# Performance work log

Hardware: AMD Instinct MI355X
Metric: run time of the kernel (lower is better)

Reference implementation:

```python
import jax, jax.numpy as jnp
import numpy as np

H = W = 128
C = 256
NC = 15
BASE_SIZE = 8.0
SCALE = 4.0
RING = np.array([0, 1, 2, 5, 8, 7, 6, 3])  # clockwise ring of 3x3 kernel (row-major idx)
BIAS_CLS = float(-np.log((1.0 - 0.01) / 0.01))  # bias_init_with_prob(0.01)


def conv(x, w, b, pad):
    y = jax.lax.conv_general_dilated(x, w, (1, 1), [(pad, pad), (pad, pad)],
                                     dimension_numbers=('NCHW', 'OIHW', 'NCHW'))
    return y + b[None, :, None, None]


def conv_relu(x, w, b):
    return jax.nn.relu(conv(x, w, b, 1))


def gen_grid_anchors(h, w, stride):
    # AnchorGeneratorRotated: base anchor centered at 0.5*(base_size-1), shifted by stride grid
    ctr = 0.5 * (BASE_SIZE - 1.0)
    gx = jnp.arange(w, dtype=jnp.float32) * stride
    gy = jnp.arange(h, dtype=jnp.float32) * stride
    yy, xx = jnp.meshgrid(gy, gx, indexing='ij')  # row-major (y outer, x inner)
    size = BASE_SIZE * SCALE
    return jnp.stack([xx + ctr, yy + ctr,
                      jnp.full_like(xx, size), jnp.full_like(xx, size),
                      jnp.zeros_like(xx)], axis=-1).reshape(-1, 5)


def norm_angle(a):
    PI = np.pi
    return ((a + PI / 4.0) % PI) - PI / 4.0  # into [-pi/4, 3pi/4)


def rboxes_decode(anchors, deltas, wh_ratio_clip=1e-6):
    # anchors [HW,5], deltas [N,HW,5] -> [N,HW,5]
    max_ratio = float(np.abs(np.log(wh_ratio_clip)))
    dx, dy, dw, dh, dt = [deltas[..., i] for i in range(5)]
    dw = jnp.clip(dw, -max_ratio, max_ratio)
    dh = jnp.clip(dh, -max_ratio, max_ratio)
    ax, ay, aw, ah, aa = [anchors[..., i] for i in range(5)]
    cos, sin = jnp.cos(aa), jnp.sin(aa)
    gx = dx * aw * cos - dy * ah * sin + ax
    gy = dx * aw * sin + dy * ah * cos + ay
    gw = aw * jnp.exp(dw)
    gh = ah * jnp.exp(dh)
    ga = norm_angle(aa + dt)
    return jnp.stack([gx, gy, gw, gh, ga], axis=-1)


def bilinear_sample(x, ys, xs):
    # x [N,C,H,W]; ys/xs [N,H,W,K] float pixel coords -> [N,C,H,W,K], zero outside
    N, Cc, h, w = x.shape
    K = ys.shape[-1]
    x0 = jnp.floor(xs)
    y0 = jnp.floor(ys)
    wx1 = xs - x0
    wx0 = 1.0 - wx1
    wy1 = ys - y0
    wy0 = 1.0 - wy1
    xf = x.reshape(N, Cc, h * w)

    def gather(yi, wy, xi, wxx):
        valid = (yi >= 0) & (yi < h) & (xi >= 0) & (xi < w)
        yc = jnp.clip(yi, 0, h - 1).astype(jnp.int32)
        xc = jnp.clip(xi, 0, w - 1).astype(jnp.int32)
        idx = (yc * w + xc).reshape(N, -1)  # [N,H*W*K]
        v = jax.vmap(lambda xi_, ii_: jnp.take(xi_, ii_, axis=1))(xf, idx)
        v = v.reshape(N, Cc, h, w, K)
        wgt = jnp.where(valid, wy * wxx, 0.0)[:, None]  # [N,1,H,W,K]
        return v * wgt

    out = gather(y0, wy0, x0, wx0)
    out = out + gather(y0, wy0, x0 + 1.0, wx1)
    out = out + gather(y0 + 1.0, wy1, x0, wx0)
    out = out + gather(y0 + 1.0, wy1, x0 + 1.0, wx1)
    return out


def align_conv(x, refine_anchor, stride, w, b):
    # deformable 3x3 conv; sampling grid from refined rotated anchors
    N, Cc, h, ww = x.shape
    k = 3
    idx = jnp.arange(-1, 2, dtype=x.dtype)
    yy, xx = jnp.meshgrid(idx, idx, indexing='ij')
    xx = xx.reshape(-1)
    yy = yy.reshape(-1)  # [9] kernel offsets, row-major matching OIHW flatten
    axc, ayc, aw, ah, aa = [refine_anchor[..., i] for i in range(5)]
    s = jnp.asarray(stride, x.dtype)
    axc, ayc, aw, ah = axc / s, ayc / s, aw / s, ah / s
    cos, sin = jnp.cos(aa), jnp.sin(aa)
    dx = (aw / k)[..., None] * xx  # [N,h,w,9]
    dy = (ah / k)[..., None] * yy
    xs = cos[..., None] * dx - sin[..., None] * dy + axc[..., None]
    ys = sin[..., None] * dx + cos[..., None] * dy + ayc[..., None]
    sampled = bilinear_sample(x, ys, xs)  # [N,C,h,w,9]
    out = jnp.einsum('nchwk,ock->nohw', sampled, w.reshape(w.shape[0], Cc, 9))
    return jax.nn.relu(out + b[None, :, None, None])


def or_conv(x, w, b):
    # ORConv2d(256->32, arf_config=(1,8)): 8 spatially-rotated copies of each 3x3 filter
    o, ci = w.shape[0], w.shape[1]
    wf = w.reshape(o, ci, 9)
    rotated = []
    for r in range(8):
        src = np.arange(9)
        for j in range(8):
            src[RING[j]] = RING[(j - r) % 8]  # rotate ring by r*45deg, center fixed
        rotated.append(wf[..., src])
    wr = jnp.stack(rotated, axis=1).reshape(o * 8, ci, 3, 3)  # channel = o*8 + r
    br = jnp.repeat(b, 8)
    return conv(x, wr, br, 1)


def setup_inputs() -> dict:
    key = jax.random.key(0)
    ks = iter(jax.random.split(key, 32))
    d = {}
    d['feats'] = jax.random.normal(next(ks), (1, C, H, W), dtype=jnp.float32)
    def wlike(shape):
        return 0.01 * jax.random.normal(next(ks), shape, dtype=jnp.float32)
    d['fam_reg_w0'] = wlike((C, C, 3, 3)); d['fam_reg_b0'] = jnp.zeros((C,), jnp.float32)
    d['fam_reg_w1'] = wlike((C, C, 3, 3)); d['fam_reg_b1'] = jnp.zeros((C,), jnp.float32)
    d['fam_reg_hw'] = wlike((5, C, 1, 1)); d['fam_reg_hb'] = jnp.zeros((5,), jnp.float32)
    d['fam_cls_w0'] = wlike((C, C, 3, 3)); d['fam_cls_b0'] = jnp.zeros((C,), jnp.float32)
    d['fam_cls_w1'] = wlike((C, C, 3, 3)); d['fam_cls_b1'] = jnp.zeros((C,), jnp.float32)
    d['fam_cls_hw'] = wlike((NC, C, 1, 1)); d['fam_cls_hb'] = jnp.full((NC,), BIAS_CLS, jnp.float32)
    d['align_w'] = wlike((C, C, 3, 3)); d['align_b'] = jnp.zeros((C,), jnp.float32)
    d['or_w'] = wlike((C // 8, C, 3, 3)); d['or_b'] = jnp.zeros((C // 8,), jnp.float32)
    d['odm_reg_w0'] = wlike((C, C, 3, 3)); d['odm_reg_b0'] = jnp.zeros((C,), jnp.float32)
    d['odm_reg_w1'] = wlike((C, C, 3, 3)); d['odm_reg_b1'] = jnp.zeros((C,), jnp.float32)
    d['odm_reg_hw'] = wlike((5, C, 3, 3)); d['odm_reg_hb'] = jnp.zeros((5,), jnp.float32)
    d['odm_cls_w0'] = wlike((C, C // 8, 3, 3)); d['odm_cls_b0'] = jnp.zeros((C,), jnp.float32)
    d['odm_cls_w1'] = wlike((C, C, 3, 3)); d['odm_cls_b1'] = jnp.zeros((C,), jnp.float32)
    d['odm_cls_hw'] = wlike((NC, C, 3, 3)); d['odm_cls_hb'] = jnp.full((NC,), BIAS_CLS, jnp.float32)
    d['stride'] = 8
    return d


def reference(feats, fam_reg_w0, fam_reg_b0, fam_reg_w1, fam_reg_b1, fam_reg_hw, fam_reg_hb,
              fam_cls_w0, fam_cls_b0, fam_cls_w1, fam_cls_b1, fam_cls_hw, fam_cls_hb,
              align_w, align_b, or_w, or_b,
              odm_reg_w0, odm_reg_b0, odm_reg_w1, odm_reg_b1, odm_reg_hw, odm_reg_hb,
              odm_cls_w0, odm_cls_b0, odm_cls_w1, odm_cls_b1, odm_cls_hw, odm_cls_hb,
              stride):
    x = feats
    t = conv_relu(conv_relu(x, fam_reg_w0, fam_reg_b0), fam_reg_w1, fam_reg_b1)
    fam_bbox_pred = conv(t, fam_reg_hw, fam_reg_hb, 0)  # [N,5,h,w]
    t = conv_relu(conv_relu(x, fam_cls_w0, fam_cls_b0), fam_cls_w1, fam_cls_b1)
    fam_cls_pred = conv(t, fam_cls_hw, fam_cls_hb, 0)   # [N,NC,h,w]
    N, _, h, w = fam_bbox_pred.shape
    anchors = gen_grid_anchors(h, w, stride)  # [h*w,5]
    deltas = jax.lax.stop_gradient(fam_bbox_pred).transpose(0, 2, 3, 1).reshape(N, -1, 5)
    refine_anchor = rboxes_decode(anchors, deltas).reshape(N, h, w, 5)
    al = align_conv(x, refine_anchor, stride, align_w, align_b)  # [N,256,h,w]
    orf = or_conv(al, or_w, or_b)                                # [N,256,h,w]
    pooled = orf.reshape(N, -1, 8, h, w).max(axis=2)             # rotation-invariant pooling -> [N,32,h,w]
    t = conv_relu(conv_relu(pooled, odm_cls_w0, odm_cls_b0), odm_cls_w1, odm_cls_b1)
    odm_cls_pred = conv(t, odm_cls_hw, odm_cls_hb, 1)
    t = conv_relu(conv_relu(orf, odm_reg_w0, odm_reg_b0), odm_reg_w1, odm_reg_b1)
    odm_bbox_pred = conv(t, odm_reg_hw, odm_reg_hb, 1)
    return (fam_cls_pred, fam_bbox_pred, odm_cls_pred, odm_bbox_pred, anchors, refine_anchor)
```

## Files before the change

kernel.cpp:

```cpp
#include <hip/hip_runtime.h>
#include <hip/hip_bf16.h>
#include <hip/hip_fp16.h>

#define HW 128
#define NPX 16384
#define CC 256

typedef short  bf16x8  __attribute__((ext_vector_type(8)));
typedef short  short4v __attribute__((ext_vector_type(4)));
typedef float  f32x4   __attribute__((ext_vector_type(4)));
typedef unsigned int u32x4 __attribute__((ext_vector_type(4)));

static __device__ __forceinline__ short f2bs(float v) {
    union { float f; unsigned u; } x; x.f = v;
    unsigned r = x.u + 0x7FFFu + ((x.u >> 16) & 1u);
    return (short)(r >> 16);
}
static __device__ __forceinline__ float bs2f(short s) {
    union { unsigned u; float f; } x; x.u = ((unsigned)(unsigned short)s) << 16;
    return x.f;
}

struct F8 { unsigned char b; };
__device__ __forceinline__ unsigned char enc8(float v) {
// ... 63 lines not shown
    }
}

__global__ __launch_bounds__(256) void v10_prep(
    const float* __restrict__ w, const float* __restrict__ bias,
    short* __restrict__ wb, float* __restrict__ bb,
    int Cout, int Cin, int OCP, int mode)
{
    int g = blockIdx.x * 256 + threadIdx.x;
    if (g < OCP) bb[g] = (g < Cout) ? ((mode == 1) ? bias[g >> 3] : bias[g]) : 0.f;
    int tot = 9 * OCP * Cin;
    if (g >= tot) return;
    int t   = g / (OCP * Cin);
    int rem = g - t * OCP * Cin;
    int oc  = rem / Cin;
    int ci  = rem - oc * Cin;
    float v = 0.f;
    if (oc < Cout) {
        if (mode == 0)      v = w[((size_t)oc * Cin + ci) * 9 + t];
        else if (mode == 1) { int o = oc >> 3, r = oc & 7;
                              v = w[((size_t)o * Cin + ci) * 9 + c_ROT9[r][t]]; }
        else if (t == 4)    v = w[(size_t)oc * Cin + ci];
    }
    wb[g] = f2bs(v);
}

__constant__ int c_JOB[14][5] = {
    {0,       256, 256, 256, 0},
    {589824,  256, 256, 256, 0},
    {1179648, 256, 256, 256, 0},
    {1769472, 256, 256, 256, 0},
    {2359296, 256, 256, 256, 0},
    {2949120, 256, 256, 256, 1},
    {3538944, 256, 256, 256, 0},
    {4128768, 256, 256, 256, 0},
    {4718592, 256, 256, 256, 0},
    {5308416, 5,   256, 64,  2},
    {5455872, 15,  256, 64,  2},
    {5603328, 5,   256, 64,  0},
    {5750784, 15,  256, 64,  0},
    {5898240, 256, 32,  256, 0},
};

__global__ __launch_bounds__(256) void v12_prepall(
    const float* w0, const float* w1, const float* w2, const float* w3,
    const float* w4, const float* w5, const float* w6, const float* w7,
    const float* w8, const float* w9, const float* w10, const float* w11,
    const float* w12, const float* w13,
    const float* b0, const float* b1, const float* b2, const float* b3,
    const float* b4, const float* b5, const float* b6, const float* b7,
    const float* b8, const float* b9, const float* b10, const float* b11,
    const float* b12, const float* b13,
    short* __restrict__ wball, float* __restrict__ bball)
{
    const float* ws_[14] = {w0,w1,w2,w3,w4,w5,w6,w7,w8,w9,w10,w11,w12,w13};
    const float* bs_[14] = {b0,b1,b2,b3,b4,b5,b6,b7,b8,b9,b10,b11,b12,b13};
    const int j = blockIdx.y;
    const int dst  = c_JOB[j][0];
    const int Cout = c_JOB[j][1];
    const int Cin  = c_JOB[j][2];
    const int OCP  = c_JOB[j][3];
    const int mode = c_JOB[j][4];
    const float* w = ws_[j];
    const float* bias = bs_[j];
    int g = blockIdx.x * 256 + threadIdx.x;
    if (g < OCP) bball[j * 256 + g] = (g < Cout) ? ((mode == 1) ? bias[g >> 3] : bias[g]) : 0.f;
    int tot = 9 * OCP * Cin;
    if (g >= tot) return;
    int t   = g / (OCP * Cin);
    int rem = g - t * OCP * Cin;
    int oc  = rem / Cin;
    int ci  = rem - oc * Cin;
    float v = 0.f;
    if (oc < Cout) {
        if (mode == 0)      v = w[((size_t)oc * Cin + ci) * 9 + t];
        else if (mode == 1) { int o = oc >> 3, r = oc & 7;
                              v = w[((size_t)o * Cin + ci) * 9 + c_ROT9[r][t]]; }
        else if (t == 4)    v = w[(size_t)oc * Cin + ci];
    }
    wball[dst + g] = f2bs(v);
}

template <int RELU, int HEAD, int ONLY1, int CIN, int OCG>
__global__ __launch_bounds__(256) void v12_conv(
    const short* __restrict__ xin, const short* __restrict__ wb,
    const float* __restrict__ bb, void* __restrict__ outv, int CoutAct)
{
    const int OCP  = gridDim.y * 64 * OCG;
    const int y    = blockIdx.x >> 1;
    const int xh   = (blockIdx.x & 1) * 64;
    const int ocb  = blockIdx.y * 64 * OCG;
    const int tid  = threadIdx.x;
    const int wv   = tid >> 6;
    const int lane = tid & 63;
    const int quad = lane >> 4;
    const int l15  = lane & 15;
    const int ocw  = ocb + wv * 16 * OCG;

    __shared__ short S[2][3 * 66 * 40];

    int gofs[4], lofs[4];
#pragma unroll
    for (int i = 0; i < 4; ++i) {
        int e = tid + i * 256;
        gofs[i] = -1; lofs[i] = -1;
        if (e < 792) {
            int pos = e >> 2, part = e & 3;
            int r = pos / 66, c = pos - r * 66;
            int yy = y - 1 + r, xx = xh - 1 + c;
            lofs[i] = (r * 66 + c) * 40 + part * 8;
            if (yy >= 0 && yy < HW && xx >= 0 && xx < HW)
                gofs[i] = (yy * HW + xx) * CIN + part * 8;
        }
    }
    const bf16x8 zf = (bf16x8){0, 0, 0, 0, 0, 0, 0, 0};

    f32x4 acc[4][OCG];
#pragma unroll
    for (int p = 0; p < 4; ++p)
#pragma unroll
        for (int g = 0; g < OCG; ++g) acc[p][g] = (f32x4){0.f, 0.f, 0.f, 0.f};

    {
        bf16x8 st[4];
#pragma unroll
        for (int i = 0; i < 4; ++i) {
            st[i] = zf;
            if (gofs[i] >= 0) st[i] = *(const bf16x8*)(xin + gofs[i]);
        }
#pragma unroll
        for (int i = 0; i < 4; ++i)
            if (lofs[i] >= 0) *(bf16x8*)(&S[0][lofs[i]]) = st[i];
    }
    __syncthreads();

    const int NST = CIN / 32;
    int cur = 0;
    for (int s = 0; s < NST; ++s) {
        const int cib = s * 32;

        bf16x8 a[9][OCG];
#pragma unroll
        for (int t = (ONLY1 ? 4 : 0); t < (ONLY1 ? 5 : 9); ++t)
#pragma unroll
            for (int g = 0; g < OCG; ++g)
                a[t][g] = *(const bf16x8*)(wb +
                    ((size_t)(t * OCP + ocw + g * 16 + l15) * CIN + cib + quad * 8));

        bf16x8 st[4];
        if (s + 1 < NST) {
#pragma unroll
            for (int i = 0; i < 4; ++i) {
                st[i] = zf;
                if (gofs[i] >= 0)
                    st[i] = *(const bf16x8*)(xin + gofs[i] + cib + 32);
            }
        }

#pragma unroll
        for (int t = (ONLY1 ? 4 : 0); t < (ONLY1 ? 5 : 9); ++t) {
            const int r = t / 3, dxk = t % 3 - 1;
#pragma unroll
            for (int p = 0; p < 4; ++p) {
                int c = 1 + p * 16 + l15 + dxk;
                bf16x8 b = *(const bf16x8*)(&S[cur][(r * 66 + c) * 40 + quad * 8]);
#pragma unroll
                for (int g = 0; g < OCG; ++g)
                    acc[p][g] = __builtin_amdgcn_mfma_f32_16x16x32_bf16(a[t][g], b, acc[p][g], 0, 0, 0);
            }
        }

        if (s + 1 < NST) {
#pragma unroll
            for (int i = 0; i < 4; ++i)
                if (lofs[i] >= 0) *(bf16x8*)(&S[cur ^ 1][lofs[i]]) = st[i];
        }
        __syncthreads();
        cur ^= 1;
    }

#pragma unroll
    for (int p = 0; p < 4; ++p) {
        const int px = y * HW + xh + p * 16 + l15;
#pragma unroll
        for (int g = 0; g < OCG; ++g) {
            const int ocq = ocw + g * 16 + quad * 4;
            if (HEAD) {
                float* o = (float*)outv;
#pragma unroll
                for (int r = 0; r < 4; ++r)
                    if (ocq + r < CoutAct)
                        o[(size_t)(ocq + r) * NPX + px] = acc[p][g][r] + bb[ocq + r];
            } else {
                short4v s4;
#pragma unroll
                for (int r = 0; r < 4; ++r) {
                    float v = acc[p][g][r] + bb[ocq + r];
                    if (RELU) v = fmaxf(v, 0.f);
                    s4[r] = f2bs(v);
                }
                *(short4v*)((short*)outv + (size_t)px * 256 + ocq) = s4;
            }
        }
    }
}

__global__ __launch_bounds__(256) void v11_align(
    const short* __restrict__ xt, const float* __restrict__ bbox,
    const short* __restrict__ wb, const float* __restrict__ bb,
    const int* __restrict__ stride_p, short* __restrict__ outa)
{
    const int y    = blockIdx.x >> 1;
    const int xh   = (blockIdx.x & 1) * 64;
    const int ocb  = blockIdx.y * 128;
    const int tid  = threadIdx.x;
    const int wv   = tid >> 6, lane = tid & 63, quad = lane >> 4, l15 = lane & 15;
    const int ocw  = ocb + wv * 32;

    __shared__ int   s_idx[4][576];
    __shared__ float s_wgt[4][576];
    __shared__ short S[2][64 * 40];

    const float s = (float)(*stride_p);
    for (int e = tid; e < 576; e += 256) {
        int t = e >> 6, xi = e & 63;
        int px = y * HW + xh + xi;
        float gx, gy, gw, gh, ga;
        v9_decode_px(bbox, px, s, gx, gy, gw, gh, ga);
        float axc = gx / s, ayc = gy / s;
        float aw3 = gw / (3.f * s), ah3 = gh / (3.f * s);
        float cs = cosf(ga), sn = sinf(ga);
        float kx = (float)(t % 3 - 1), ky = (float)(t / 3 - 1);
        float ddx = aw3 * kx, ddy = ah3 * ky;
        float xf = cs * ddx - sn * ddy + axc;
        float yf = sn * ddx + cs * ddy + ayc;
        float fx = floorf(xf), fy = floorf(yf);
        int ix = (int)fx, iy = (int)fy;
        float wx1 = xf - fx, wx0 = 1.f - wx1;
        float wy1 = yf - fy, wy0 = 1.f - wy1;
        bool x0v = (ix >= 0) && (ix < HW), x1v = (ix + 1 >= 0) && (ix + 1 < HW);
        bool y0v = (iy >= 0) && (iy < HW), y1v = (iy + 1 >= 0) && (iy + 1 < HW);
        int x0c = min(max(ix, 0), HW - 1), x1c = min(max(ix + 1, 0), HW - 1);
        int y0c = min(max(iy, 0), HW - 1), y1c = min(max(iy + 1, 0), HW - 1);
        s_idx[0][e] = y0c * HW + x0c;
        s_idx[1][e] = y0c * HW + x1c;
        s_idx[2][e] = y1c * HW + x0c;
        s_idx[3][e] = y1c * HW + x1c;
        s_wgt[0][e] = (y0v && x0v) ? wy0 * wx0 : 0.f;
        s_wgt[1][e] = (y0v && x1v) ? wy0 * wx1 : 0.f;
        s_wgt[2][e] = (y1v && x0v) ? wy1 * wx0 : 0.f;
        s_wgt[3][e] = (y1v && x1v) ? wy1 * wx1 : 0.f;
    }

    f32x4 acc[4][2];
#pragma unroll
    for (int p = 0; p < 4; ++p) { acc[p][0] = (f32x4){0,0,0,0}; acc[p][1] = (f32x4){0,0,0,0}; }

    const int spx = tid >> 2;
    const int sq  = tid & 3;
    const int sw  = spx * 40 + sq * 8;
    const bf16x8 zf = (bf16x8){0, 0, 0, 0, 0, 0, 0, 0};

    __syncthreads();

    bf16x8 a0, a1;
    {
        int e = spx;
        int i0 = s_idx[0][e], i1 = s_idx[1][e], i2 = s_idx[2][e], i3 = s_idx[3][e];
        float w0 = s_wgt[0][e], w1 = s_wgt[1][e], w2 = s_wgt[2][e], w3 = s_wgt[3][e];
        const short* base = xt + sq * 8;
        bf16x8 g0 = *(const bf16x8*)(base + (size_t)i0 * 256);
        bf16x8 g1 = *(const bf16x8*)(base + (size_t)i1 * 256);
        bf16x8 g2 = *(const bf16x8*)(base + (size_t)i2 * 256);
        bf16x8 g3 = *(const bf16x8*)(base + (size_t)i3 * 256);
        a0 = *(const bf16x8*)(wb + ((size_t)(0 * 256 + ocw + l15) * 256 + 0 + quad * 8));
        a1 = *(const bf16x8*)(wb + ((size_t)(0 * 256 + ocw + 16 + l15) * 256 + 0 + quad * 8));
        float v[8];
#pragma unroll
        for (int i = 0; i < 8; ++i)
            v[i] = w0 * bs2f(g0[i]) + w1 * bs2f(g1[i]) + w2 * bs2f(g2[i]) + w3 * bs2f(g3[i]);
        u32x4 r;
#pragma unroll
        for (int i = 0; i < 4; ++i)
            asm("v_cvt_pk_bf16_f32 %0, %1, %2" : "=v"(r[i]) : "v"(v[2 * i]), "v"(v[2 * i + 1]));
        *(u32x4*)(&S[0][sw]) = r;
    }
    __syncthreads();

    int cur = 0;
    for (int cib = 0; cib < 256; cib += 32) {
        for (int t = 0; t < 9; ++t) {
            const bool last = (cib == 224) && (t == 8);
            const int nt   = (t == 8) ? 0 : t + 1;
            const int ncib = (t == 8) ? cib + 32 : cib;

            bf16x8 ng0 = zf, ng1 = zf, ng2 = zf, ng3 = zf;
            bf16x8 na0 = a0, na1 = a1;
            float nw0 = 0.f, nw1 = 0.f, nw2 = 0.f, nw3 = 0.f;
            if (!last) {
                int e = nt * 64 + spx;
                int i0 = s_idx[0][e], i1 = s_idx[1][e], i2 = s_idx[2][e], i3 = s_idx[3][e];
                nw0 = s_wgt[0][e]; nw1 = s_wgt[1][e]; nw2 = s_wgt[2][e]; nw3 = s_wgt[3][e];
                const short* base = xt + ncib + sq * 8;
                ng0 = *(const bf16x8*)(base + (size_t)i0 * 256);
                ng1 = *(const bf16x8*)(base + (size_t)i1 * 256);
                ng2 = *(const bf16x8*)(base + (size_t)i2 * 256);
                ng3 = *(const bf16x8*)(base + (size_t)i3 * 256);
                na0 = *(const bf16x8*)(wb + ((size_t)(nt * 256 + ocw + l15) * 256 + ncib + quad * 8));
                na1 = *(const bf16x8*)(wb + ((size_t)(nt * 256 + ocw + 16 + l15) * 256 + ncib + quad * 8));
            }

#pragma unroll
            for (int p = 0; p < 4; ++p) {
                bf16x8 b = *(const bf16x8*)(&S[cur][(p * 16 + l15) * 40 + quad * 8]);
                acc[p][0] = __builtin_amdgcn_mfma_f32_16x16x32_bf16(a0, b, acc[p][0], 0, 0, 0);
                acc[p][1] = __builtin_amdgcn_mfma_f32_16x16x32_bf16(a1, b, acc[p][1], 0, 0, 0);
            }

            if (!last) {
                float v[8];
#pragma unroll
                for (int i = 0; i < 8; ++i)
                    v[i] = nw0 * bs2f(ng0[i]) + nw1 * bs2f(ng1[i])
                         + nw2 * bs2f(ng2[i]) + nw3 * bs2f(ng3[i]);
                u32x4 r;
#pragma unroll
                for (int i = 0; i < 4; ++i)
                    asm("v_cvt_pk_bf16_f32 %0, %1, %2" : "=v"(r[i]) : "v"(v[2 * i]), "v"(v[2 * i + 1]));
                *(u32x4*)(&S[cur ^ 1][sw]) = r;
            }
            a0 = na0; a1 = na1;
            cur ^= 1;
            __syncthreads();
        }
    }

#pragma unroll
    for (int p = 0; p < 4; ++p) {
        const int px = y * HW + xh + p * 16 + l15;
#pragma unroll
        for (int g = 0; g < 2; ++g) {
            const int ocq = ocw + g * 16 + quad * 4;
            short4v s4;
#pragma unroll
            for (int r = 0; r < 4; ++r)
                s4[r] = f2bs(fmaxf(acc[p][g][r] + bb[ocq + r], 0.f));
            *(short4v*)(outa + (size_t)px * 256 + ocq) = s4;
        }
    }
}

__global__ __launch_bounds__(256) void v10_pool(
    const short* __restrict__ t1, short* __restrict__ p)
{
    int g = blockIdx.x * 256 + threadIdx.x;
    if (g >= 32 * NPX) return;
    int px = g >> 5, c = g & 31;
    const short* q = t1 + (size_t)px * 256 + c * 8;
    float m = bs2f(q[0]);
#pragma unroll
    for (int r = 1; r < 8; ++r) m = fmaxf(m, bs2f(q[r]));
    p[(size_t)px * 32 + c] = f2bs(m);
}

__global__ __launch_bounds__(256) void v9_decode(
    const float* __restrict__ bbox, float* __restrict__ anchors_out,
    float* __restrict__ refine_out, const int* __restrict__ stride_p)
{
    int px = blockIdx.x * 256 + threadIdx.x;
    if (px >= NPX) return;
    float s = (float)(*stride_p);
    int y = px >> 7, x = px & 127;
    anchors_out[px * 5 + 0] = x * s + 3.5f;
    anchors_out[px * 5 + 1] = y * s + 3.5f;
    anchors_out[px * 5 + 2] = 32.f;
    anchors_out[px * 5 + 3] = 32.f;
    anchors_out[px * 5 + 4] = 0.f;
    float gx, gy, gw, gh, ga;
    v9_decode_px(bbox, px, s, gx, gy, gw, gh, ga);
    refine_out[px * 5 + 0] = gx;
    refine_out[px * 5 + 1] = gy;
    refine_out[px * 5 + 2] = gw;
    refine_out[px * 5 + 3] = gh;
    refine_out[px * 5 + 4] = ga;
}

template <typename TIN, int RELU, int ORCONV>
__global__ __launch_bounds__(256) void v9_conv3x3(
    const TIN* __restrict__ in, const float* __restrict__ w,
    const float* __restrict__ bias, F8* __restrict__ out, int Cin)
{
    const int y   = blockIdx.x;
    const int ocb = blockIdx.y * 64;
    const int tid = threadIdx.x;
    const int xg  = tid & 15;
    const int og  = tid >> 4;
    const int x0  = xg * 8;
    const int oc0 = ocb + og * 4;

    __shared__ float srow[3][132];
    float acc[4][8];
#pragma unroll
    for (int i = 0; i < 4; ++i)
#pragma unroll
        for (int j = 0; j < 8; ++j) acc[i][j] = 0.f;

    for (int ci = 0; ci < Cin; ++ci) {
        __syncthreads();
        const TIN* inp = in + (size_t)ci * NPX;
        for (int t = tid; t < 3 * 130; t += 256) {
            int r = t / 130, c = t - r * 130;
            int yy = y - 1 + r, xx = c - 1;
            float v = 0.f;
            if (yy >= 0 && yy < HW && xx >= 0 && xx < HW) v = ldg_(inp + yy * HW + xx);
// ... 141 lines not shown
            bool yv1 = (iy + 1 >= 0) && (iy + 1 < HW);
            if (yv0 && xv0) v += ip[iy * HW + ix] * wy0 * wx0;
            if (yv0 && xv1) v += ip[iy * HW + ix + 1] * wy0 * wx1;
            if (yv1 && xv0) v += ip[(iy + 1) * HW + ix] * wy1 * wx0;
            if (yv1 && xv1) v += ip[(iy + 1) * HW + ix + 1] * wy1 * wx1;
            smp[t >> 7][t & 127] = v;
        }
        __syncthreads();

        float wv[4][9];
#pragma unroll
        for (int i = 0; i < 4; ++i) {
            const float* wp = w + ((size_t)(oc0 + i) * CC + ci) * 9;
#pragma unroll
            for (int k = 0; k < 9; ++k) wv[i][k] = wp[k];
        }
#pragma unroll
        for (int k = 0; k < 9; ++k) {
            float iv[8];
#pragma unroll
            for (int j = 0; j < 8; ++j) iv[j] = smp[k][x0 + j];
#pragma unroll
            for (int i = 0; i < 4; ++i)
#pragma unroll
                for (int j = 0; j < 8; ++j)
                    acc[i][j] += iv[j] * wv[i][k];
        }
    }
#pragma unroll
    for (int i = 0; i < 4; ++i) {
        float b = bias[oc0 + i];
#pragma unroll
        for (int j = 0; j < 8; ++j)
            out[(size_t)(oc0 + i) * NPX + y * HW + x0 + j].b =
                enc8(fmaxf(acc[i][j] + b, 0.f));
    }
}

__global__ __launch_bounds__(256) void v9_pool(
    const F8* __restrict__ orf, F8* __restrict__ pooled)
{
    int g = blockIdx.x * 256 + threadIdx.x;
    if (g >= 32 * NPX) return;
    int px = g & (NPX - 1);
    int c  = g >> 14;
    float m = -3.4e38f;
#pragma unroll
    for (int r = 0; r < 8; ++r)
        m = fmaxf(m, dec8(orf[(size_t)(c * 8 + r) * NPX + px]));
    pooled[g].b = enc8(m);
}

extern "C" void kernel_launch(void* const* d_in, const int* in_sizes, int n_in,
                              void* d_out, int out_size, void* d_ws, size_t ws_size,
                              hipStream_t stream)
{
    const float* feats = (const float*)d_in[0];
    const float* frw0 = (const float*)d_in[1];  const float* frb0 = (const float*)d_in[2];
    const float* frw1 = (const float*)d_in[3];  const float* frb1 = (const float*)d_in[4];
    const float* frhw = (const float*)d_in[5];  const float* frhb = (const float*)d_in[6];
    const float* fcw0 = (const float*)d_in[7];  const float* fcb0 = (const float*)d_in[8];
    const float* fcw1 = (const float*)d_in[9];  const float* fcb1 = (const float*)d_in[10];
    const float* fchw = (const float*)d_in[11]; const float* fchb = (const float*)d_in[12];
    const float* alw  = (const float*)d_in[13]; const float* alb  = (const float*)d_in[14];
    const float* orw  = (const float*)d_in[15]; const float* orb  = (const float*)d_in[16];
    const float* drw0 = (const float*)d_in[17]; const float* drb0 = (const float*)d_in[18];
    const float* drw1 = (const float*)d_in[19]; const float* drb1 = (const float*)d_in[20];
    const float* drhw = (const float*)d_in[21]; const float* drhb = (const float*)d_in[22];
    const float* dcw0 = (const float*)d_in[23]; const float* dcb0 = (const float*)d_in[24];
    const float* dcw1 = (const float*)d_in[25]; const float* dcb1 = (const float*)d_in[26];
    const float* dchw = (const float*)d_in[27]; const float* dchb = (const float*)d_in[28];
    const int*  stride_p = (const int*)d_in[29];

    float* out = (float*)d_out;
    float* o_fam_cls  = out;
    float* o_fam_bbox = out + 245760;
    float* o_odm_cls  = out + 327680;
    float* o_odm_bbox = out + 573440;
    float* o_anchors  = out + 655360;
    float* o_refine   = out + 737280;

    dim3 blk(256);

    const size_t NEED2     = 38172672;
    const size_t NEED_FAST = 27395072;
    const size_t NEED_V9   = 8912896;

    if (ws_size >= NEED2) {
        char* ws = (char*)d_ws;
        short* xt = (short*)(ws + 0);
        short* T0 = (short*)(ws + 8388608);
        short* T1 = (short*)(ws + 16777216);
        short* P  = (short*)(ws + 25165824);
        short* WA = (short*)(ws + 26214400);
        float* BA = (float*)(ws + 38158336);

        dim3 gc(256, 2), gh(256, 1);

        v12_prepall<<<dim3(2304, 14), blk, 0, stream>>>(
            frw0, frw1, fcw0, fcw1, alw, orw, drw0, drw1, dcw1,
            frhw, fchw, drhw, dchw, dcw0,
            frb0, frb1, fcb0, fcb1, alb, orb, drb0, drb1, dcb1,
            frhb, fchb, drhb, dchb, dcb0,
            WA, BA);
        v10_transpose<<<dim3(512, 8), blk, 0, stream>>>(feats, xt);

        v12_conv<1, 0, 0, 256, 2><<<gc, blk, 0, stream>>>(xt, WA + 0,       BA + 0 * 256, T0, 256);
        v12_conv<1, 0, 0, 256, 2><<<gc, blk, 0, stream>>>(T0, WA + 589824,  BA + 1 * 256, T1, 256);
        v12_conv<0, 1, 1, 256, 1><<<gh, blk, 0, stream>>>(T1, WA + 5308416, BA + 9 * 256, o_fam_bbox, 5);
        v12_conv<1, 0, 0, 256, 2><<<gc, blk, 0, stream>>>(xt, WA + 1179648, BA + 2 * 256, T0, 256);
        v12_conv<1, 0, 0, 256, 2><<<gc, blk, 0, stream>>>(T0, WA + 1769472, BA + 3 * 256, T1, 256);
        v12_conv<0, 1, 1, 256, 1><<<gh, blk, 0, stream>>>(T1, WA + 5455872, BA + 10 * 256, o_fam_cls, 15);
        v9_decode<<<dim3(64), blk, 0, stream>>>(o_fam_bbox, o_anchors, o_refine, stride_p);
        v11_align<<<dim3(256, 2), blk, 0, stream>>>(xt, o_fam_bbox, WA + 2359296, BA + 4 * 256, stride_p, T0);
        v12_conv<0, 0, 0, 256, 2><<<gc, blk, 0, stream>>>(T0, WA + 2949120, BA + 5 * 256, T1, 256);
        v10_pool<<<dim3(2048), blk, 0, stream>>>(T1, P);
        v12_conv<1, 0, 0, 256, 2><<<gc, blk, 0, stream>>>(T1, WA + 3538944, BA + 6 * 256, T0, 256);
        v12_conv<1, 0, 0, 256, 2><<<gc, blk, 0, stream>>>(T0, WA + 4128768, BA + 7 * 256, T1, 256);
        v12_conv<0, 1, 0, 256, 1><<<gh, blk, 0, stream>>>(T1, WA + 5603328, BA + 11 * 256, o_odm_bbox, 5);
        v12_conv<1, 0, 0, 32, 2><<<gc, blk, 0, stream>>>(P, WA + 5898240, BA + 13 * 256, T0, 256);
        v12_conv<1, 0, 0, 256, 2><<<gc, blk, 0, stream>>>(T0, WA + 4718592, BA + 8 * 256, T1, 256);
        v12_conv<0, 1, 0, 256, 1><<<gh, blk, 0, stream>>>(T1, WA + 5750784, BA + 12 * 256, o_odm_cls, 15);
    } else if (ws_size >= NEED_FAST) {
        char* ws = (char*)d_ws;
        short* xt = (short*)(ws + 0);
        short* T0 = (short*)(ws + 8388608);
        short* T1 = (short*)(ws + 16777216);
        short* P  = (short*)(ws + 25165824);
        short* WB = (short*)(ws + 26214400);
        float* BB = (float*)(ws + 27394048);

        dim3 gc(256, 2), gh(256, 1);

        v10_transpose<<<dim3(512, 8), blk, 0, stream>>>(feats, xt);

#define PREP(W, B, COUT, CIN, OCP, MODE) \
        v10_prep<<<dim3((9 * (OCP) * (CIN) + 255) / 256), blk, 0, stream>>>( \
            W, B, WB, BB, COUT, CIN, OCP, MODE)

        PREP(frw0, frb0, 256, 256, 256, 0);
        v12_conv<1, 0, 0, 256, 2><<<gc, blk, 0, stream>>>(xt, WB, BB, T0, 256);
        PREP(frw1, frb1, 256, 256, 256, 0);
        v12_conv<1, 0, 0, 256, 2><<<gc, blk, 0, stream>>>(T0, WB, BB, T1, 256);
        PREP(frhw, frhb, 5, 256, 64, 2);
        v12_conv<0, 1, 1, 256, 1><<<gh, blk, 0, stream>>>(T1, WB, BB, o_fam_bbox, 5);
        PREP(fcw0, fcb0, 256, 256, 256, 0);
        v12_conv<1, 0, 0, 256, 2><<<gc, blk, 0, stream>>>(xt, WB, BB, T0, 256);
        PREP(fcw1, fcb1, 256, 256, 256, 0);
        v12_conv<1, 0, 0, 256, 2><<<gc, blk, 0, stream>>>(T0, WB, BB, T1, 256);
        PREP(fchw, fchb, 15, 256, 64, 2);
        v12_conv<0, 1, 1, 256, 1><<<gh, blk, 0, stream>>>(T1, WB, BB, o_fam_cls, 15);
        v9_decode<<<dim3(64), blk, 0, stream>>>(o_fam_bbox, o_anchors, o_refine, stride_p);
        PREP(alw, alb, 256, 256, 256, 0);
        v11_align<<<dim3(256, 2), blk, 0, stream>>>(xt, o_fam_bbox, WB, BB, stride_p, T0);
        PREP(orw, orb, 256, 256, 256, 1);
        v12_conv<0, 0, 0, 256, 2><<<gc, blk, 0, stream>>>(T0, WB, BB, T1, 256);
        v10_pool<<<dim3(2048), blk, 0, stream>>>(T1, P);
        PREP(drw0, drb0, 256, 256, 256, 0);
        v12_conv<1, 0, 0, 256, 2><<<gc, blk, 0, stream>>>(T1, WB, BB, T0, 256);
        PREP(drw1, drb1, 256, 256, 256, 0);
        v12_conv<1, 0, 0, 256, 2><<<gc, blk, 0, stream>>>(T0, WB, BB, T1, 256);
        PREP(drhw, drhb, 5, 256, 64, 0);
        v12_conv<0, 1, 0, 256, 1><<<gh, blk, 0, stream>>>(T1, WB, BB, o_odm_bbox, 5);
        PREP(dcw0, dcb0, 256, 32, 256, 0);
        v12_conv<1, 0, 0, 32, 2><<<gc, blk, 0, stream>>>(P, WB, BB, T0, 256);
        PREP(dcw1, dcb1, 256, 256, 256, 0);
        v12_conv<1, 0, 0, 256, 2><<<gc, blk, 0, stream>>>(T0, WB, BB, T1, 256);
        PREP(dchw, dchb, 15, 256, 64, 0);
        v12_conv<0, 1, 0, 256, 1><<<gh, blk, 0, stream>>>(T1, WB, BB, o_odm_cls, 15);
#undef PREP
    } else if (ws_size >= NEED_V9) {
        F8* A = (F8*)d_ws;
        F8* B = (F8*)((char*)d_ws + 4194304);
        F8* P = (F8*)((char*)d_ws + 8388608);
        dim3 gconv(128, 4);

        v9_conv3x3<float, 1, 0><<<gconv, blk, 0, stream>>>(feats, frw0, frb0, A, 256);
        v9_conv3x3<F8,    1, 0><<<gconv, blk, 0, stream>>>(A, frw1, frb1, B, 256);
        v9_head1x1<<<dim3(5 * 64), blk, 0, stream>>>(B, frhw, frhb, o_fam_bbox, 5);
        v9_conv3x3<float, 1, 0><<<gconv, blk, 0, stream>>>(feats, fcw0, fcb0, A, 256);
        v9_conv3x3<F8,    1, 0><<<gconv, blk, 0, stream>>>(A, fcw1, fcb1, B, 256);
        v9_head1x1<<<dim3(15 * 64), blk, 0, stream>>>(B, fchw, fchb, o_fam_cls, 15);
        v9_decode<<<dim3(64), blk, 0, stream>>>(o_fam_bbox, o_anchors, o_refine, stride_p);
        v9_align<<<gconv, blk, 0, stream>>>(feats, o_fam_bbox, alw, alb, stride_p, A);
        v9_conv3x3<F8, 0, 1><<<gconv, blk, 0, stream>>>(A, orw, orb, B, 256);
        v9_pool<<<dim3(2048), blk, 0, stream>>>(B, P);
        v9_conv3x3<F8, 1, 0><<<gconv, blk, 0, stream>>>(B, drw0, drb0, A, 256);
        v9_conv3x3<F8, 1, 0><<<gconv, blk, 0, stream>>>(A, drw1, drb1, B, 256);
        v9_head3x3<<<dim3(5 * 64), blk, 0, stream>>>(B, drhw, drhb, o_odm_bbox, 5);
        v9_conv3x3<F8, 1, 0><<<gconv, blk, 0, stream>>>(P, dcw0, dcb0, A, 32);
        v9_conv3x3<F8, 1, 0><<<gconv, blk, 0, stream>>>(A, dcw1, dcb1, B, 256);
        v9_head3x3<<<dim3(15 * 64), blk, 0, stream>>>(B, dchw, dchb, o_odm_cls, 15);
    }
}
```

Before: 601.2 us.

## Pair independent conv branches into joint launches and prefetch weights across stages

Adds a paired conv kernel that runs two independent branches (reg/cls towers) in one launch by splitting blockIdx.y, which doubles the grid per launch and halves the launch count when a larger workspace is available. The conv body now prefetches the next stage's weights right after each tap's MFMAs, so weights are no longer reloaded at the top of every stage. The align kernel deepens its gather prefetch to two steps ahead. This costs more registers and extra workspace buffers, and the new path only runs if the workspace is at least the new threshold.

```diff
diff --git a/kernel.cpp b/kernel.cpp
--- a/kernel.cpp
+++ b/kernel.cpp
@@ -169,22 +169,21 @@
 }
 
 template <int RELU, int HEAD, int ONLY1, int CIN, int OCG>
-__global__ __launch_bounds__(256) void v12_conv(
+__device__ __forceinline__ void conv_body(
+    short* S,
     const short* __restrict__ xin, const short* __restrict__ wb,
-    const float* __restrict__ bb, void* __restrict__ outv, int CoutAct)
-{
-    const int OCP  = gridDim.y * 64 * OCG;
-    const int y    = blockIdx.x >> 1;
-    const int xh   = (blockIdx.x & 1) * 64;
-    const int ocb  = blockIdx.y * 64 * OCG;
+    const float* __restrict__ bb, void* __restrict__ outv,
+    int CoutAct, int OCP, int bx, int oy)
+{
+    const int y    = bx >> 1;
+    const int xh   = (bx & 1) * 64;
+    const int ocb  = oy * 64 * OCG;
     const int tid  = threadIdx.x;
     const int wv   = tid >> 6;
     const int lane = tid & 63;
     const int quad = lane >> 4;
     const int l15  = lane & 15;
     const int ocw  = ocb + wv * 16 * OCG;
-
-    __shared__ short S[2][3 * 66 * 40];
 
     int gofs[4], lofs[4];
 #pragma unroll
@@ -217,22 +216,21 @@
         }
 #pragma unroll
         for (int i = 0; i < 4; ++i)
-            if (lofs[i] >= 0) *(bf16x8*)(&S[0][lofs[i]]) = st[i];
-    }
+            if (lofs[i] >= 0) *(bf16x8*)(&S[lofs[i]]) = st[i];
+    }
+    bf16x8 a[9][OCG];
+#pragma unroll
+    for (int t = (ONLY1 ? 4 : 0); t < (ONLY1 ? 5 : 9); ++t)
+#pragma unroll
+        for (int g = 0; g < OCG; ++g)
+            a[t][g] = *(const bf16x8*)(wb +
+                ((size_t)(t * OCP + ocw + g * 16 + l15) * CIN + quad * 8));
     __syncthreads();
 
     const int NST = CIN / 32;
     int cur = 0;
     for (int s = 0; s < NST; ++s) {
         const int cib = s * 32;
-
-        bf16x8 a[9][OCG];
-#pragma unroll
-        for (int t = (ONLY1 ? 4 : 0); t < (ONLY1 ? 5 : 9); ++t)
-#pragma unroll
-            for (int g = 0; g < OCG; ++g)
-                a[t][g] = *(const bf16x8*)(wb +
-                    ((size_t)(t * OCP + ocw + g * 16 + l15) * CIN + cib + quad * 8));
 
         bf16x8 st[4];
         if (s + 1 < NST) {
@@ -250,17 +248,23 @@
 #pragma unroll
             for (int p = 0; p < 4; ++p) {
                 int c = 1 + p * 16 + l15 + dxk;
-                bf16x8 b = *(const bf16x8*)(&S[cur][(r * 66 + c) * 40 + quad * 8]);
+                bf16x8 b = *(const bf16x8*)(&S[cur * 7920 + (r * 66 + c) * 40 + quad * 8]);
 #pragma unroll
                 for (int g = 0; g < OCG; ++g)
                     acc[p][g] = __builtin_amdgcn_mfma_f32_16x16x32_bf16(a[t][g], b, acc[p][g], 0, 0, 0);
             }
+            if (s + 1 < NST) {
+#pragma unroll
+                for (int g = 0; g < OCG; ++g)
+                    a[t][g] = *(const bf16x8*)(wb +
+                        ((size_t)(t * OCP + ocw + g * 16 + l15) * CIN + cib + 32 + quad * 8));
+            }
         }
 
         if (s + 1 < NST) {
 #pragma unroll
             for (int i = 0; i < 4; ++i)
-                if (lofs[i] >= 0) *(bf16x8*)(&S[cur ^ 1][lofs[i]]) = st[i];
+                if (lofs[i] >= 0) *(bf16x8*)(&S[(cur ^ 1) * 7920 + lofs[i]]) = st[i];
         }
         __syncthreads();
         cur ^= 1;
@@ -292,7 +296,36 @@
     }
 }
 
-__global__ __launch_bounds__(256) void v11_align(
+template <int RELU, int HEAD, int ONLY1, int CIN, int OCG>
+__global__ __launch_bounds__(256) void v13_conv(
+    const short* __restrict__ xin, const short* __restrict__ wb,
+    const float* __restrict__ bb, void* __restrict__ outv,
+    int CoutAct, int OCP)
+{
+    __shared__ short S[2 * 7920];
+    conv_body<RELU, HEAD, ONLY1, CIN, OCG>(S, xin, wb, bb, outv,
+                                           CoutAct, OCP, blockIdx.x, blockIdx.y);
+}
+
+template <int RELU, int HEAD, int ONLY1, int CIN0, int CIN1, int OCG, int NY, int OCP>
+__global__ __launch_bounds__(256) void v13_pair(
+    const short* __restrict__ in0, const short* __restrict__ in1,
+    const short* __restrict__ wb0, const short* __restrict__ wb1,
+    const float* __restrict__ bb0, const float* __restrict__ bb1,
+    void* __restrict__ out0, void* __restrict__ out1,
+    int cout0, int cout1)
+{
+    __shared__ short S[2 * 7920];
+    const int ybr = blockIdx.y;
+    if (ybr < NY)
+        conv_body<RELU, HEAD, ONLY1, CIN0, OCG>(S, in0, wb0, bb0, out0,
+                                                cout0, OCP, blockIdx.x, ybr);
+    else
+        conv_body<RELU, HEAD, ONLY1, CIN1, OCG>(S, in1, wb1, bb1, out1,
+                                                cout1, OCP, blockIdx.x, ybr - NY);
+}
+
+__global__ __launch_bounds__(256) void v13_align(
     const short* __restrict__ xt, const float* __restrict__ bbox,
     const short* __restrict__ wb, const float* __restrict__ bb,
     const int* __restrict__ stride_p, short* __restrict__ outa)
@@ -350,7 +383,9 @@
 
     __syncthreads();
 
-    bf16x8 a0, a1;
+    bf16x8 aC0, aC1;
+    bf16x8 gN0, gN1, gN2, gN3;
+    float  wN0, wN1, wN2, wN3;
     {
         int e = spx;
         int i0 = s_idx[0][e], i1 = s_idx[1][e], i2 = s_idx[2][e], i3 = s_idx[3][e];
@@ -360,8 +395,6 @@
         bf16x8 g1 = *(const bf16x8*)(base + (size_t)i1 * 256);
         bf16x8 g2 = *(const bf16x8*)(base + (size_t)i2 * 256);
         bf16x8 g3 = *(const bf16x8*)(base + (size_t)i3 * 256);
-        a0 = *(const bf16x8*)(wb + ((size_t)(0 * 256 + ocw + l15) * 256 + 0 + quad * 8));
-        a1 = *(const bf16x8*)(wb + ((size_t)(0 * 256 + ocw + 16 + l15) * 256 + 0 + quad * 8));
         float v[8];
 #pragma unroll
         for (int i = 0; i < 8; ++i)
@@ -372,51 +405,70 @@
             asm("v_cvt_pk_bf16_f32 %0, %1, %2" : "=v"(r[i]) : "v"(v[2 * i]), "v"(v[2 * i + 1]));
         *(u32x4*)(&S[0][sw]) = r;
     }
+    {
+        int e = 64 + spx;
+        int i0 = s_idx[0][e], i1 = s_idx[1][e], i2 = s_idx[2][e], i3 = s_idx[3][e];
+        wN0 = s_wgt[0][e]; wN1 = s_wgt[1][e]; wN2 = s_wgt[2][e]; wN3 = s_wgt[3][e];
+        const short* base = xt + sq * 8;
+        gN0 = *(const bf16x8*)(base + (size_t)i0 * 256);
+        gN1 = *(const bf16x8*)(base + (size_t)i1 * 256);
+        gN2 = *(const bf16x8*)(base + (size_t)i2 * 256);
+        gN3 = *(const bf16x8*)(base + (size_t)i3 * 256);
+    }
+    aC0 = *(const bf16x8*)(wb + ((size_t)(ocw + l15) * 256 + quad * 8));
+    aC1 = *(const bf16x8*)(wb + ((size_t)(ocw + 16 + l15) * 256 + quad * 8));
     __syncthreads();
 
     int cur = 0;
     for (int cib = 0; cib < 256; cib += 32) {
         for (int t = 0; t < 9; ++t) {
-            const bool last = (cib == 224) && (t == 8);
-            const int nt   = (t == 8) ? 0 : t + 1;
-            const int ncib = (t == 8) ? cib + 32 : cib;
-
-            bf16x8 ng0 = zf, ng1 = zf, ng2 = zf, ng3 = zf;
-            bf16x8 na0 = a0, na1 = a1;
-            float nw0 = 0.f, nw1 = 0.f, nw2 = 0.f, nw3 = 0.f;
-            if (!last) {
-                int e = nt * 64 + spx;
+            const bool have1 = !(cib == 224 && t == 8);
+            const bool have2 = !(cib == 224 && t >= 7);
+            const int t1 = (t == 8) ? 0 : t + 1;
+            const int c1 = (t == 8) ? cib + 32 : cib;
+            int t2 = t + 2, c2 = cib;
+            if (t2 > 8) { t2 -= 9; c2 += 32; }
+
+            bf16x8 gF0 = zf, gF1 = zf, gF2 = zf, gF3 = zf;
+            float  wF0 = 0.f, wF1 = 0.f, wF2 = 0.f, wF3 = 0.f;
+            if (have2) {
+                int e = t2 * 64 + spx;
                 int i0 = s_idx[0][e], i1 = s_idx[1][e], i2 = s_idx[2][e], i3 = s_idx[3][e];
-                nw0 = s_wgt[0][e]; nw1 = s_wgt[1][e]; nw2 = s_wgt[2][e]; nw3 = s_wgt[3][e];
-                const short* base = xt + ncib + sq * 8;
-                ng0 = *(const bf16x8*)(base + (size_t)i0 * 256);
-                ng1 = *(const bf16x8*)(base + (size_t)i1 * 256);
-                ng2 = *(const bf16x8*)(base + (size_t)i2 * 256);
-                ng3 = *(const bf16x8*)(base + (size_t)i3 * 256);
-                na0 = *(const bf16x8*)(wb + ((size_t)(nt * 256 + ocw + l15) * 256 + ncib + quad * 8));
-                na1 = *(const bf16x8*)(wb + ((size_t)(nt * 256 + ocw + 16 + l15) * 256 + ncib + quad * 8));
+                wF0 = s_wgt[0][e]; wF1 = s_wgt[1][e]; wF2 = s_wgt[2][e]; wF3 = s_wgt[3][e];
+                const short* base = xt + c2 + sq * 8;
+                gF0 = *(const bf16x8*)(base + (size_t)i0 * 256);
+                gF1 = *(const bf16x8*)(base + (size_t)i1 * 256);
+                gF2 = *(const bf16x8*)(base + (size_t)i2 * 256);
+                gF3 = *(const bf16x8*)(base + (size_t)i3 * 256);
+            }
+            bf16x8 aN0 = aC0, aN1 = aC1;
+            if (have1) {
+                aN0 = *(const bf16x8*)(wb + ((size_t)(t1 * 256 + ocw + l15) * 256 + c1 + quad * 8));
+                aN1 = *(const bf16x8*)(wb + ((size_t)(t1 * 256 + ocw + 16 + l15) * 256 + c1 + quad * 8));
             }
 
 #pragma unroll
             for (int p = 0; p < 4; ++p) {
                 bf16x8 b = *(const bf16x8*)(&S[cur][(p * 16 + l15) * 40 + quad * 8]);
-                acc[p][0] = __builtin_amdgcn_mfma_f32_16x16x32_bf16(a0, b, acc[p][0], 0, 0, 0);
-                acc[p][1] = __builtin_amdgcn_mfma_f32_16x16x32_bf16(a1, b, acc[p][1], 0, 0, 0);
+                acc[p][0] = __builtin_amdgcn_mfma_f32_16x16x32_bf16(aC0, b, acc[p][0], 0, 0, 0);
+                acc[p][1] = __builtin_amdgcn_mfma_f32_16x16x32_bf16(aC1, b, acc[p][1], 0, 0, 0);
             }
 
-            if (!last) {
+            if (have1) {
                 float v[8];
 #pragma unroll
                 for (int i = 0; i < 8; ++i)
-                    v[i] = nw0 * bs2f(ng0[i]) + nw1 * bs2f(ng1[i])
-                         + nw2 * bs2f(ng2[i]) + nw3 * bs2f(ng3[i]);
+                    v[i] = wN0 * bs2f(gN0[i]) + wN1 * bs2f(gN1[i])
+                         + wN2 * bs2f(gN2[i]) + wN3 * bs2f(gN3[i]);
                 u32x4 r;
 #pragma unroll
                 for (int i = 0; i < 4; ++i)
                     asm("v_cvt_pk_bf16_f32 %0, %1, %2" : "=v"(r[i]) : "v"(v[2 * i]), "v"(v[2 * i + 1]));
                 *(u32x4*)(&S[cur ^ 1][sw]) = r;
             }
-            a0 = na0; a1 = na1;
+            gN0 = gF0; gN1 = gF1; gN2 = gF2; gN3 = gF3;
+            wN0 = wF0; wN1 = wF1; wN2 = wF2; wN3 = wF3;
+            aC0 = aN0; aC1 = aN1;
             cur ^= 1;
             __syncthreads();
         }
@@ -724,11 +776,49 @@
 
     dim3 blk(256);
 
+    const size_t NEED3     = 55097344;
     const size_t NEED2     = 38172672;
     const size_t NEED_FAST = 27395072;
     const size_t NEED_V9   = 8912896;
 
-    if (ws_size >= NEED2) {
+    if (ws_size >= NEED3) {
+        char* ws = (char*)d_ws;
+        short* xt = (short*)(ws + 0);
+        short* T0 = (short*)(ws + 8388608);
+        short* T1 = (short*)(ws + 16777216);
+        short* T2 = (short*)(ws + 25165824);
+        short* T3 = (short*)(ws + 33554432);
+        short* P  = (short*)(ws + 41943040);
+        short* WA = (short*)(ws + 42991616);
+        float* BA = (float*)(ws + 55083008);
+
+        v12_prepall<<<dim3(2304, 14), blk, 0, stream>>>(
+            frw0, frw1, fcw0, fcw1, alw, orw, drw0, drw1, dcw1,
+            frhw, fchw, drhw, dchw, dcw0,
+            frb0, frb1, fcb0, fcb1, alb, orb, drb0, drb1, dcb1,
+            frhb, fchb, drhb, dchb, dcb0,
+            WA, BA);
+        v10_transpose<<<dim3(512, 8), blk, 0, stream>>>(feats, xt);
+
+        v13_pair<1, 0, 0, 256, 256, 2, 2, 256><<<dim3(256, 4), blk, 0, stream>>>(
+            xt, xt, WA + 0, WA + 1179648, BA + 0 * 256, BA + 2 * 256, T0, T2, 256, 256);
+        v13_pair<1, 0, 0, 256, 256, 2, 2, 256><<<dim3(256, 4), blk, 0, stream>>>(
+            T0, T2, WA + 589824, WA + 1769472, BA + 1 * 256, BA + 3 * 256, T1, T3, 256, 256);
+        v13_pair<0, 1, 1, 256, 256, 1, 1, 64><<<dim3(256, 2), blk, 0, stream>>>(
+            T1, T3, WA + 5308416, WA + 5455872, BA + 9 * 256, BA + 10 * 256,
+            o_fam_bbox, o_fam_cls, 5, 15);
+        v9_decode<<<dim3(64), blk, 0, stream>>>(o_fam_bbox, o_anchors, o_refine, stride_p);
+        v13_align<<<dim3(256, 2), blk, 0, stream>>>(xt, o_fam_bbox, WA + 2359296, BA + 4 * 256, stride_p, T0);
+        v13_conv<0, 0, 0, 256, 2><<<dim3(256, 2), blk, 0, stream>>>(T0, WA + 2949120, BA + 5 * 256, T1, 256, 256);
+        v10_pool<<<dim3(2048), blk, 0, stream>>>(T1, P);
+        v13_pair<1, 0, 0, 256, 32, 2, 2, 256><<<dim3(256, 4), blk, 0, stream>>>(
+            T1, P, WA + 3538944, WA + 5898240, BA + 6 * 256, BA + 13 * 256, T0, T2, 256, 256);
+        v13_pair<1, 0, 0, 256, 256, 2, 2, 256><<<dim3(256, 4), blk, 0, stream>>>(
+            T0, T2, WA + 4128768, WA + 4718592, BA + 7 * 256, BA + 8 * 256, T1, T3, 256, 256);
+        v13_pair<0, 1, 0, 256, 256, 1, 1, 64><<<dim3(256, 2), blk, 0, stream>>>(
+            T1, T3, WA + 5603328, WA + 5750784, BA + 11 * 256, BA + 12 * 256,
+            o_odm_bbox, o_odm_cls, 5, 15);
+    } else if (ws_size >= NEED2) {
         char* ws = (char*)d_ws;
         short* xt = (short*)(ws + 0);
         short* T0 = (short*)(ws + 8388608);
@@ -747,22 +837,22 @@
             WA, BA);
         v10_transpose<<<dim3(512, 8), blk, 0, stream>>>(feats, xt);
 
-        v12_conv<1, 0, 0, 256, 2><<<gc, blk, 0, stream>>>(xt, WA + 0,       BA + 0 * 256, T0, 256);
-        v12_conv<1, 0, 0, 256, 2><<<gc, blk, 0, stream>>>(T0, WA + 589824,  BA + 1 * 256, T1, 256);
-        v12_conv<0, 1, 1, 256, 1><<<gh, blk, 0, stream>>>(T1, WA + 5308416, BA + 9 * 256, o_fam_bbox, 5);
-        v12_conv<1, 0, 0, 256, 2><<<gc, blk, 0, stream>>>(xt, WA + 1179648, BA + 2 * 256, T0, 256);
-        v12_conv<1, 0, 0, 256, 2><<<gc, blk, 0, stream>>>(T0, WA + 1769472, BA + 3 * 256, T1, 256);
-        v12_conv<0, 1, 1, 256, 1><<<gh, blk, 0, stream>>>(T1, WA + 5455872, BA + 10 * 256, o_fam_cls, 15);
+        v13_conv<1, 0, 0, 256, 2><<<gc, blk, 0, stream>>>(xt, WA + 0,       BA + 0 * 256, T0, 256, 256);
+        v13_conv<1, 0, 0, 256, 2><<<gc, blk, 0, stream>>>(T0, WA + 589824,  BA + 1 * 256, T1, 256, 256);
+        v13_conv<0, 1, 1, 256, 1><<<gh, blk, 0, stream>>>(T1, WA + 5308416, BA + 9 * 256, o_fam_bbox, 5, 64);
+        v13_conv<1, 0, 0, 256, 2><<<gc, blk, 0, stream>>>(xt, WA + 1179648, BA + 2 * 256, T0, 256, 256);
+        v13_conv<1, 0, 0, 256, 2><<<gc, blk, 0, stream>>>(T0, WA + 1769472, BA + 3 * 256, T1, 256, 256);
+        v13_conv<0, 1, 1, 256, 1><<<gh, blk, 0, stream>>>(T1, WA + 5455872, BA + 10 * 256, o_fam_cls, 15, 64);
         v9_decode<<<dim3(64), blk, 0, stream>>>(o_fam_bbox, o_anchors, o_refine, stride_p);
-        v11_align<<<dim3(256, 2), blk, 0, stream>>>(xt, o_fam_bbox, WA + 2359296, BA + 4 * 256, stride_p, T0);
-        v12_conv<0, 0, 0, 256, 2><<<gc, blk, 0, stream>>>(T0, WA + 2949120, BA + 5 * 256, T1, 256);
+        v13_align<<<dim3(256, 2), blk, 0, stream>>>(xt, o_fam_bbox, WA + 2359296, BA + 4 * 256, stride_p, T0);
+        v13_conv<0, 0, 0, 256, 2><<<gc, blk, 0, stream>>>(T0, WA + 2949120, BA + 5 * 256, T1, 256, 256);
         v10_pool<<<dim3(2048), blk, 0, stream>>>(T1, P);
-        v12_conv<1, 0, 0, 256, 2><<<gc, blk, 0, stream>>>(T1, WA + 3538944, BA + 6 * 256, T0, 256);
-        v12_conv<1, 0, 0, 256, 2><<<gc, blk, 0, stream>>>(T0, WA + 4128768, BA + 7 * 256, T1, 256);
-        v12_conv<0, 1, 0, 256, 1><<<gh, blk, 0, stream>>>(T1, WA + 5603328, BA + 11 * 256, o_odm_bbox, 5);
-        v12_conv<1, 0, 0, 32, 2><<<gc, blk, 0, stream>>>(P, WA + 5898240, BA + 13 * 256, T0, 256);
-        v12_conv<1, 0, 0, 256, 2><<<gc, blk, 0, stream>>>(T0, WA + 4718592, BA + 8 * 256, T1, 256);
-        v12_conv<0, 1, 0, 256, 1><<<gh, blk, 0, stream>>>(T1, WA + 5750784, BA + 12 * 256, o_odm_cls, 15);
+        v13_conv<1, 0, 0, 256, 2><<<gc, blk, 0, stream>>>(T1, WA + 3538944, BA + 6 * 256, T0, 256, 256);
+        v13_conv<1, 0, 0, 256, 2><<<gc, blk, 0, stream>>>(T0, WA + 4128768, BA + 7 * 256, T1, 256, 256);
+        v13_conv<0, 1, 0, 256, 1><<<gh, blk, 0, stream>>>(T1, WA + 5603328, BA + 11 * 256, o_odm_bbox, 5, 64);
+        v13_conv<1, 0, 0, 32, 2><<<gc, blk, 0, stream>>>(P, WA + 5898240, BA + 13 * 256, T0, 256, 256);
+        v13_conv<1, 0, 0, 256, 2><<<gc, blk, 0, stream>>>(T0, WA + 4718592, BA + 8 * 256, T1, 256, 256);
+        v13_conv<0, 1, 0, 256, 1><<<gh, blk, 0, stream>>>(T1, WA + 5750784, BA + 12 * 256, o_odm_cls, 15, 64);
     } else if (ws_size >= NEED_FAST) {
         char* ws = (char*)d_ws;
         short* xt = (short*)(ws + 0);
@@ -781,35 +871,35 @@
             W, B, WB, BB, COUT, CIN, OCP, MODE)
 
         PREP(frw0, frb0, 256, 256, 256, 0);
-        v12_conv<1, 0, 0, 256, 2><<<gc, blk, 0, stream>>>(xt, WB, BB, T0, 256);
+        v13_conv<1, 0, 0, 256, 2><<<gc, blk, 0, stream>>>(xt, WB, BB, T0, 256, 256);
         PREP(frw1, frb1, 256, 256, 256, 0);
-        v12_conv<1, 0, 0, 256, 2><<<gc, blk, 0, stream>>>(T0, WB, BB, T1, 256);
+        v13_conv<1, 0, 0, 256, 2><<<gc, blk, 0, stream>>>(T0, WB, BB, T1, 256, 256);
         PREP(frhw, frhb, 5, 256, 64, 2);
-        v12_conv<0, 1, 1, 256, 1><<<gh, blk, 0, stream>>>(T1, WB, BB, o_fam_bbox, 5);
+        v13_conv<0, 1, 1, 256, 1><<<gh, blk, 0, stream>>>(T1, WB, BB, o_fam_bbox, 5, 64);
         PREP(fcw0, fcb0, 256, 256, 256, 0);
-        v12_conv<1, 0, 0, 256, 2><<<gc, blk, 0, stream>>>(xt, WB, BB, T0, 256);
+        v13_conv<1, 0, 0, 256, 2><<<gc, blk, 0, stream>>>(xt, WB, BB, T0, 256, 256);
         PREP(fcw1, fcb1, 256, 256, 256, 0);
-        v12_conv<1, 0, 0, 256, 2><<<gc, blk, 0, stream>>>(T0, WB, BB, T1, 256);
+        v13_conv<1, 0, 0, 256, 2><<<gc, blk, 0, stream>>>(T0, WB, BB, T1, 256, 256);
         PREP(fchw, fchb, 15, 256, 64, 2);
-        v12_conv<0, 1, 1, 256, 1><<<gh, blk, 0, stream>>>(T1, WB, BB, o_fam_cls, 15);
+        v13_conv<0, 1, 1, 256, 1><<<gh, blk, 0, stream>>>(T1, WB, BB, o_fam_cls, 15, 64);
         v9_decode<<<dim3(64), blk, 0, stream>>>(o_fam_bbox, o_anchors, o_refine, stride_p);
         PREP(alw, alb, 256, 256, 256, 0);
-        v11_align<<<dim3(256, 2), blk, 0, stream>>>(xt, o_fam_bbox, WB, BB, stride_p, T0);
+        v13_align<<<dim3(256, 2), blk, 0, stream>>>(xt, o_fam_bbox, WB, BB, stride_p, T0);
         PREP(orw, orb, 256, 256, 256, 1);
-        v12_conv<0, 0, 0, 256, 2><<<gc, blk, 0, stream>>>(T0, WB, BB, T1, 256);
+        v13_conv<0, 0, 0, 256, 2><<<gc, blk, 0, stream>>>(T0, WB, BB, T1, 256, 256);
         v10_pool<<<dim3(2048), blk, 0, stream>>>(T1, P);
         PREP(drw0, drb0, 256, 256, 256, 0);
-        v12_conv<1, 0, 0, 256, 2><<<gc, blk, 0, stream>>>(T1, WB, BB, T0, 256);
+        v13_conv<1, 0, 0, 256, 2><<<gc, blk, 0, stream>>>(T1, WB, BB, T0, 256, 256);
         PREP(drw1, drb1, 256, 256, 256, 0);
-        v12_conv<1, 0, 0, 256, 2><<<gc, blk, 0, stream>>>(T0, WB, BB, T1, 256);
+        v13_conv<1, 0, 0, 256, 2><<<gc, blk, 0, stream>>>(T0, WB, BB, T1, 256, 256);
         PREP(drhw, drhb, 5, 256, 64, 0);
-        v12_conv<0, 1, 0, 256, 1><<<gh, blk, 0, stream>>>(T1, WB, BB, o_odm_bbox, 5);
+        v13_conv<0, 1, 0, 256, 1><<<gh, blk, 0, stream>>>(T1, WB, BB, o_odm_bbox, 5, 64);
         PREP(dcw0, dcb0, 256, 32, 256, 0);
-        v12_conv<1, 0, 0, 32, 2><<<gc, blk, 0, stream>>>(P, WB, BB, T0, 256);
+        v13_conv<1, 0, 0, 32, 2><<<gc, blk, 0, stream>>>(P, WB, BB, T0, 256, 256);
         PREP(dcw1, dcb1, 256, 256, 256, 0);
-        v12_conv<1, 0, 0, 256, 2><<<gc, blk, 0, stream>>>(T0, WB, BB, T1, 256);
+        v13_conv<1, 0, 0, 256, 2><<<gc, blk, 0, stream>>>(T0, WB, BB, T1, 256, 256);
         PREP(dchw, dchb, 15, 256, 64, 0);
-        v12_conv<0, 1, 0, 256, 1><<<gh, blk, 0, stream>>>(T1, WB, BB, o_odm_cls, 15);
+        v13_conv<0, 1, 0, 256, 1><<<gh, blk, 0, stream>>>(T1, WB, BB, o_odm_cls, 15, 64);
 #undef PREP
     } else if (ws_size >= NEED_V9) {
         F8* A = (F8*)d_ws;
```

Result: faster. 562.4 us (-6.5%).
